# Optimization experiments

Measured on AMD Instinct MI355X. Metric: run time of the kernel, lower is better.

Reference implementation:

```python
import jax, jax.numpy as jnp
import numpy as np

N, E, D, O = 50000, 800000, 128, 128
BN_EPS = 1e-5

def setup_inputs() -> dict:
    key = jax.random.key(0)
    ks = jax.random.split(key, 12)
    s1 = 1.0 / np.sqrt(D)
    s2 = 1.0 / np.sqrt(O)
    return {
        "x": jax.random.normal(ks[0], (N, D), dtype=jnp.float32),
        "edge_index": jax.random.randint(ks[1], (2, E), 0, N, dtype=jnp.int64),
        "batch": jnp.zeros((N,), dtype=jnp.int64),
        "eps": jnp.float32(0.0),  # GINConv train_eps parameter, init 0
        "W1": jax.random.uniform(ks[2], (O, D), jnp.float32, -s1, s1),
        "b1": jax.random.uniform(ks[3], (O,), jnp.float32, -s1, s1),
        "gamma1": jnp.ones((O,), jnp.float32),
        "beta1": jnp.zeros((O,), jnp.float32),
        "W2": jax.random.uniform(ks[4], (O, O), jnp.float32, -s2, s2),
        "b2": jax.random.uniform(ks[5], (O,), jnp.float32, -s2, s2),
        "gamma2": jnp.ones((O,), jnp.float32),
        "beta2": jnp.zeros((O,), jnp.float32),
    }

def _bn(h, gamma, beta):
    # BatchNorm1d training mode: biased variance over nodes
    m = jnp.mean(h, axis=0)
    v = jnp.var(h, axis=0)
    return (h - m) * jax.lax.rsqrt(v + BN_EPS) * gamma + beta

def reference(x, edge_index, batch, eps, W1, b1, gamma1, beta1, W2, b2, gamma2, beta2):
    src, dst = edge_index[0], edge_index[1]
    # sum_{j in N(i)} x_j  (scatter-add over edges)
    agg = jax.ops.segment_sum(x[src], dst, num_segments=N)
    h = (1.0 + eps) * x + agg
    h = jax.nn.relu(_bn(h @ W1.T + b1, gamma1, beta1))
    h = jax.nn.relu(_bn(h @ W2.T + b2, gamma2, beta2))
    return h
```

## Files before the change

kernel.cpp:

```cpp
#include <hip/hip_runtime.h>
#include <hip/hip_bf16.h>

typedef __hip_bfloat16 bf16;
typedef unsigned short u16;
typedef unsigned int u32;
typedef __attribute__((ext_vector_type(8))) short short8;
typedef __attribute__((ext_vector_type(4))) float floatx4;

#define N_NODES 50000
#define N_EDGES 800000
#define DIM 128
#define NB2 1563
#define NB2A 1792
#define CAP2 768
#define T_EDGES 4096
#define NT1 196
#define XCHUNKS 3125
#define WROW 136
#define WIMG (128 * WROW)

__device__ __forceinline__ u16 f2bfbits(float f) {
    bf16 h = __float2bfloat16(f);
    return *(u16*)&h;
}
__device__ __forceinline__ unsigned pack2(float a, float b) {
    return (unsigned)f2bfbits(a) | ((unsigned)f2bfbits(b) << 16);
}
__device__ __forceinline__ float lo2f(u32 u) { u32 v = u << 16; return __builtin_bit_cast(float, v); }
__device__ __forceinline__ float hi2f(u32 u) { u32 v = u & 0xFFFF0000u; return __builtin_bit_cast(float, v); }
__device__ __forceinline__ float b162f(u16 u) { u32 v = (u32)u << 16; return __builtin_bit_cast(float, v); }

__launch_bounds__(256)
__global__ void k1_kernel(const float* __restrict__ x, const int* __restrict__ ei,
                          u32* __restrict__ xb,
                          const float* __restrict__ W1, const float* __restrict__ W2,
                          u16* __restrict__ w1i, u16* __restrict__ w2i,
                          u32* __restrict__ gbuck, int* __restrict__ gcur) {
    __shared__ int hist[NB2A];
    __shared__ int cur[NB2A];
    __shared__ int gbase[NB2A];
    __shared__ int sdet;
    int t = threadIdx.x, bid = blockIdx.x;

    if (bid < NT1) {
        if (t == 0) sdet = 0;
        for (int i = t; i < NB2A; i += 256) { hist[i] = 0; cur[i] = 0; }
        __syncthreads();
        if (t < 64) { if (ei[2 * t + 1] != 0) atomicOr(&sdet, 1); }
        __syncthreads();
        int is64 = (sdet == 0);
        int e0 = bid * T_EDGES;
        int n = N_EDGES - e0; if (n > T_EDGES) n = T_EDGES;
        u32 ed[T_EDGES / 256];
        #pragma unroll
        for (int j = 0; j < T_EDGES / 256; j++) {
            int idx = j * 256 + t;
            if (idx < n) {
                int e = e0 + idx;
                int js = e, jd = N_EDGES + e;
                if (is64) { js = 2 * e; jd = 2 * (N_EDGES + e); }
                u32 p = (u32)ei[js] | ((u32)ei[jd] << 16);
                ed[j] = p;
                atomicAdd(&hist[p >> 21], 1);
            }
        }
        __syncthreads();
        for (int i = t; i < NB2; i += 256) {
            int c = hist[i];
            gbase[i] = c ? atomicAdd(&gcur[i * 16], c) : 0;
        }
        __syncthreads();
        #pragma unroll
        for (int j = 0; j < T_EDGES / 256; j++) {
            int idx = j * 256 + t;
            if (idx < n) {
                u32 p = ed[j];
                int b = p >> 21;
                int pos = gbase[b] + atomicAdd(&cur[b], 1);
                gbuck[(long)b * CAP2 + pos] = p;
            }
        }
    } else if (bid < NT1 + XCHUNKS) {
        int uu = bid - NT1;
        int i = (uu * 256 + t) * 8;
        floatx4 v0 = *(const floatx4*)&x[i];
        floatx4 v1 = *(const floatx4*)&x[i + 4];
        uint4 r;
        r.x = pack2(v0[0], v0[1]); r.y = pack2(v0[2], v0[3]);
        r.z = pack2(v1[0], v1[1]); r.w = pack2(v1[2], v1[3]);
        *(uint4*)&xb[i / 2] = r;
    } else {
        int which = bid - NT1 - XCHUNKS;
        const float* W = which ? W2 : W1;
        u16* wi = which ? w2i : w1i;
        #pragma unroll 4
        for (int j = 0; j < 68; j++) {
            int q = j * 256 + t;
            int r = q / WROW, c = q - r * WROW;
            wi[q] = (c < 128) ? f2bfbits(W[r * 128 + c]) : (u16)0;
        }
    }
}

__launch_bounds__(256)
__global__ void sortagg_kernel(const u32* __restrict__ xb, const u32* __restrict__ gbuck,
                               const int* __restrict__ gcur, const float* __restrict__ epsp,
                               u32* __restrict__ hw) {
    __shared__ u32 sbuf[CAP2];
    __shared__ u16 slist[CAP2];
    __shared__ int cnt[32], offs[32], cur[32];
    int t = threadIdx.x, lane = t & 63, wv = t >> 6;
    int h = lane >> 5, q = lane & 31;
    int b = blockIdx.x;
    int n = gcur[b * 16]; if (n > CAP2) n = CAP2;
    long base = (long)b * CAP2;
    const uint2* xb2 = (const uint2*)xb;

    if (t < 32) { cnt[t] = 0; cur[t] = 0; }
    __syncthreads();
    for (int i = t; i < n; i += 256) {
        u32 p = gbuck[base + i];
        sbuf[i] = p;
        atomicAdd(&cnt[(p >> 16) & 31], 1);
    }
    __syncthreads();
    if (t < 32) {
        int v = cnt[t], pv = v;
        #pragma unroll
        for (int d = 1; d < 32; d <<= 1) { int up = __shfl_up(pv, d); if (t >= d) pv += up; }
        offs[t] = pv - v;
    }
    __syncthreads();
    for (int i = t; i < n; i += 256) {
        u32 p = sbuf[i];
        int d = (p >> 16) & 31;
        int pos = offs[d] + atomicAdd(&cur[d], 1);
        slist[pos] = (u16)(p & 0xFFFF);
    }
    __syncthreads();

    float ep1 = 1.0f + epsp[0];
    for (int p = wv; p < 16; p += 4) {
        int nA = 2 * p, nB = 2 * p + 1;
        int nodeS = b * 32 + 2 * p + h;
        int sOK = nodeS < N_NODES;
        uint2 sS = xb2[(size_t)(sOK ? nodeS : 0) * 32 + q];
        int iA = offs[nA], eA = iA + cnt[nA];
        int iB = offs[nB], eB = iB + cnt[nB];
        float a0 = 0.f, a1 = 0.f, a2 = 0.f, a3 = 0.f;
        float c0 = 0.f, c1 = 0.f, c2 = 0.f, c3 = 0.f;

        while (iA + 8 <= eA && iB + 8 <= eB) {
            int mA[4], mB[4]; uint2 uA[4], uB[4];
            #pragma unroll
            for (int j = 0; j < 4; j++) { mA[j] = slist[iA + 2 * j + h]; mB[j] = slist[iB + 2 * j + h]; }
            #pragma unroll
            for (int j = 0; j < 4; j++) { uA[j] = xb2[(size_t)mA[j] * 32 + q]; uB[j] = xb2[(size_t)mB[j] * 32 + q]; }
            #pragma unroll
            for (int j = 0; j < 4; j++) {
                a0 += lo2f(uA[j].x); a1 += hi2f(uA[j].x); a2 += lo2f(uA[j].y); a3 += hi2f(uA[j].y);
                c0 += lo2f(uB[j].x); c1 += hi2f(uB[j].x); c2 += lo2f(uB[j].y); c3 += hi2f(uB[j].y);
            }
            iA += 8; iB += 8;
        }
        while (iA + 8 <= eA) {
            int mA[4]; uint2 uA[4];
            #pragma unroll
            for (int j = 0; j < 4; j++) mA[j] = slist[iA + 2 * j + h];
            #pragma unroll
            for (int j = 0; j < 4; j++) uA[j] = xb2[(size_t)mA[j] * 32 + q];
            #pragma unroll
            for (int j = 0; j < 4; j++) {
                a0 += lo2f(uA[j].x); a1 += hi2f(uA[j].x); a2 += lo2f(uA[j].y); a3 += hi2f(uA[j].y);
            }
            iA += 8;
        }
        while (iB + 8 <= eB) {
            int mB[4]; uint2 uB[4];
            #pragma unroll
            for (int j = 0; j < 4; j++) mB[j] = slist[iB + 2 * j + h];
            #pragma unroll
            for (int j = 0; j < 4; j++) uB[j] = xb2[(size_t)mB[j] * 32 + q];
            #pragma unroll
            for (int j = 0; j < 4; j++) {
                c0 += lo2f(uB[j].x); c1 += hi2f(uB[j].x); c2 += lo2f(uB[j].y); c3 += hi2f(uB[j].y);
            }
            iB += 8;
        }
        while (iA < eA || iB < eB) {
            int ia0 = iA + h, ia1 = iA + 2 + h, ib0 = iB + h, ib1 = iB + 2 + h;
            int va0 = ia0 < eA, va1 = ia1 < eA, vb0 = ib0 < eB, vb1 = ib1 < eB;
            int mA0 = slist[va0 ? ia0 : 0], mA1 = slist[va1 ? ia1 : 0];
            int mB0 = slist[vb0 ? ib0 : 0], mB1 = slist[vb1 ? ib1 : 0];
            uint2 uA0 = xb2[(size_t)mA0 * 32 + q], uA1 = xb2[(size_t)mA1 * 32 + q];
            uint2 uB0 = xb2[(size_t)mB0 * 32 + q], uB1 = xb2[(size_t)mB1 * 32 + q];
            if (va0) { a0 += lo2f(uA0.x); a1 += hi2f(uA0.x); a2 += lo2f(uA0.y); a3 += hi2f(uA0.y); }
            if (va1) { a0 += lo2f(uA1.x); a1 += hi2f(uA1.x); a2 += lo2f(uA1.y); a3 += hi2f(uA1.y); }
            if (vb0) { c0 += lo2f(uB0.x); c1 += hi2f(uB0.x); c2 += lo2f(uB0.y); c3 += hi2f(uB0.y); }
            if (vb1) { c0 += lo2f(uB1.x); c1 += hi2f(uB1.x); c2 += lo2f(uB1.y); c3 += hi2f(uB1.y); }
            iA += 4; iB += 4;
        }
        if (sOK) {
            if (h == 0) {
                a0 += ep1 * lo2f(sS.x); a1 += ep1 * hi2f(sS.x);
                a2 += ep1 * lo2f(sS.y); a3 += ep1 * hi2f(sS.y);
            } else {
                c0 += ep1 * lo2f(sS.x); c1 += ep1 * hi2f(sS.x);
                c2 += ep1 * lo2f(sS.y); c3 += ep1 * hi2f(sS.y);
            }
        }
        a0 += __shfl_xor(a0, 32); a1 += __shfl_xor(a1, 32);
        a2 += __shfl_xor(a2, 32); a3 += __shfl_xor(a3, 32);
        c0 += __shfl_xor(c0, 32); c1 += __shfl_xor(c1, 32);
        c2 += __shfl_xor(c2, 32); c3 += __shfl_xor(c3, 32);
        float r0 = h ? c0 : a0, r1 = h ? c1 : a1, r2 = h ? c2 : a2, r3 = h ? c3 : a3;
        if (sOK) {
            uint2 w; w.x = pack2(r0, r1); w.y = pack2(r2, r3);
            *(uint2*)&hw[(size_t)nodeS * 64 + 2 * q] = w;
        }
    }
}

template<int TRANSFORM>
__launch_bounds__(256)
__global__ void gemm_mfma(const u16* __restrict__ Ap, const u16* __restrict__ wimg,
                          const float* __restrict__ bias,
                          const float* __restrict__ gamma, const float* __restrict__ beta,
                          const float* __restrict__ gstat,
                          u16* __restrict__ Yp, float* __restrict__ ostat) {
    __shared__ u16 sW[WIMG];
    __shared__ float sScale[128], sShift[128], sBias[128], sSum[128], sSq[128];
    int t = threadIdx.x, lane = t & 63, wv = t >> 6;

    #pragma unroll
    for (int it = 0; it < 9; it++) {
        int q = it * 256 + t;
        if (q < WIMG / 8) *(uint4*)&sW[q * 8] = ((const uint4*)wimg)[q];
    }
    if (t < 128) {
        sSum[t] = 0.f; sSq[t] = 0.f; sBias[t] = bias[t];
        if (TRANSFORM) {
            float m = gstat[t * 16] * (1.0f / N_NODES);
            float v = fmaxf(gstat[t * 16 + 8] * (1.0f / N_NODES) - m * m, 0.0f);
            float rs = rsqrtf(v + 1e-5f);
            float sc = gamma[t] * rs;
            sScale[t] = sc;
            sShift[t] = beta[t] - m * sc;
        }
    }
    __syncthreads();

    int col0 = lane & 15, quad = lane >> 4;
    int row0 = blockIdx.x * 128 + wv * 32;

    short8 afr[2][4];
    #pragma unroll
    for (int tt = 0; tt < 2; tt++) {
        int mrow = row0 + tt * 16 + col0;
        if (mrow > N_NODES - 1) mrow = N_NODES - 1;
        #pragma unroll
        for (int ks = 0; ks < 4; ks++)
            afr[tt][ks] = *(const short8*)&Ap[mrow * DIM + ks * 32 + quad * 8];
    }
    if (TRANSFORM) {
        #pragma unroll
        for (int tt = 0; tt < 2; tt++)
            #pragma unroll
            for (int ks = 0; ks < 4; ks++) {
                int kb = ks * 32 + quad * 8;
                short8 a = afr[tt][ks], r;
                #pragma unroll
                for (int j = 0; j < 8; j++) {
                    float f = b162f((u16)a[j]);
                    r[j] = (short)f2bfbits(fmaxf(fmaf(f, sScale[kb + j], sShift[kb + j]), 0.f));
                }
                afr[tt][ks] = r;
            }
    }

    floatx4 acc[2][8];
    #pragma unroll
    for (int tt = 0; tt < 2; tt++)
        #pragma unroll
        for (int nt = 0; nt < 8; nt++) acc[tt][nt] = (floatx4){0.f, 0.f, 0.f, 0.f};
    #pragma unroll
    for (int ks = 0; ks < 4; ks++)
        #pragma unroll
        for (int nt = 0; nt < 8; nt++) {
            short8 bfr = *(const short8*)&sW[(nt * 16 + col0) * WROW + ks * 32 + quad * 8];
            acc[0][nt] = __builtin_amdgcn_mfma_f32_16x16x32_bf16(afr[0][ks], bfr, acc[0][nt], 0, 0, 0);
            acc[1][nt] = __builtin_amdgcn_mfma_f32_16x16x32_bf16(afr[1][ks], bfr, acc[1][nt], 0, 0, 0);
        }

    #pragma unroll
    for (int tt = 0; tt < 2; tt++) {
        int rtile = row0 + tt * 16;
        if (rtile >= N_NODES) break;
        #pragma unroll
        for (int nt = 0; nt < 8; nt++) {
            int col = nt * 16 + col0;
            float bb = sBias[col];
            float o0 = acc[tt][nt][0] + bb, o1 = acc[tt][nt][1] + bb;
            float o2 = acc[tt][nt][2] + bb, o3 = acc[tt][nt][3] + bb;
            int rbase = rtile + quad * 4;
            Yp[(rbase + 0) * DIM + col] = f2bfbits(o0);
            Yp[(rbase + 1) * DIM + col] = f2bfbits(o1);
            Yp[(rbase + 2) * DIM + col] = f2bfbits(o2);
            Yp[(rbase + 3) * DIM + col] = f2bfbits(o3);
            float s = o0 + o1 + o2 + o3;
            float q = o0 * o0 + o1 * o1 + o2 * o2 + o3 * o3;
            s += __shfl_xor(s, 16); s += __shfl_xor(s, 32);
            q += __shfl_xor(q, 16); q += __shfl_xor(q, 32);
            if (quad == 0) { atomicAdd(&sSum[col], s); atomicAdd(&sSq[col], q); }
        }
    }
    __syncthreads();
    if (t < 128) {
        atomicAdd(&ostat[t * 16], sSum[t]);
        atomicAdd(&ostat[t * 16 + 8], sSq[t]);
    }
}

__global__ void output_kernel(const u32* __restrict__ Y,
                              const float* __restrict__ gstat,
                              const float* __restrict__ gamma, const float* __restrict__ beta,
                              float* __restrict__ out) {
    __shared__ float sScale[128], sShift[128];
    int t = threadIdx.x;
    if (t < 128) {
        float m = gstat[t * 16] * (1.0f / N_NODES);
        float v = fmaxf(gstat[t * 16 + 8] * (1.0f / N_NODES) - m * m, 0.0f);
        float rs = rsqrtf(v + 1e-5f);
        float sc = gamma[t] * rs;
        sScale[t] = sc;
        sShift[t] = beta[t] - m * sc;
    }
    __syncthreads();
    int i = (blockIdx.x * 256 + t) * 8;
    int c = i & 127;
    uint4 v = *(const uint4*)&Y[i / 2];
    u32 w[4] = {v.x, v.y, v.z, v.w};
    floatx4 o0, o1;
    #pragma unroll
    for (int j = 0; j < 4; j++) {
        float lo = lo2f(w[j]), hi = hi2f(w[j]);
        float r0 = fmaxf(fmaf(lo, sScale[c + 2 * j],     sShift[c + 2 * j]),     0.f);
        float r1 = fmaxf(fmaf(hi, sScale[c + 2 * j + 1], sShift[c + 2 * j + 1]), 0.f);
        if (j < 2) { o0[2 * j] = r0; o0[2 * j + 1] = r1; }
        else       { o1[2 * (j - 2)] = r0; o1[2 * (j - 2) + 1] = r1; }
    }
    *(floatx4*)&out[i] = o0;
    *(floatx4*)&out[i + 4] = o1;
}

extern "C" void kernel_launch(void* const* d_in, const int* in_sizes, int n_in,
                              void* d_out, int out_size, void* d_ws, size_t ws_size,
                              hipStream_t stream) {
    const float* x   = (const float*)d_in[0];
    const int* eraw  = (const int*)d_in[1];
    const float* eps = (const float*)d_in[3];
    const float* W1  = (const float*)d_in[4];
    const float* b1  = (const float*)d_in[5];
    const float* g1  = (const float*)d_in[6];
    const float* be1 = (const float*)d_in[7];
    const float* W2  = (const float*)d_in[8];
    const float* b2  = (const float*)d_in[9];
    const float* g2  = (const float*)d_in[10];
    const float* be2 = (const float*)d_in[11];

    char* ws = (char*)d_ws;
    size_t off = 0;
    u32* xb = (u32*)(ws + off);          off += (size_t)N_NODES * DIM * 2;
    u32* h1 = (u32*)(ws + off);          off += (size_t)N_NODES * DIM * 2;
    u16* y1 = (u16*)(ws + off);          off += (size_t)N_NODES * DIM * 2;
    u16* y2 = (u16*)(ws + off);          off += (size_t)N_NODES * DIM * 2;
    float* stats = (float*)(ws + off);   off += 4096 * 4;
    float* st1 = stats;
    float* st2 = stats + 2048;
    u16* w1i = (u16*)(ws + off);         off += (size_t)WIMG * 2;
    u16* w2i = (u16*)(ws + off);         off += (size_t)WIMG * 2;
    u32* gbuck = (u32*)(ws + off);       off += (size_t)NB2 * CAP2 * 4;
    int* gcur = (int*)(ws + off);        off += (size_t)((NB2 * 16 + 255) & ~255) * 4;

    hipMemsetAsync(gcur, 0, (size_t)NB2 * 16 * 4, stream);
    hipMemsetAsync(stats, 0, 4096 * 4, stream);

    k1_kernel<<<NT1 + XCHUNKS + 2, 256, 0, stream>>>(x, eraw, xb, W1, W2, w1i, w2i, gbuck, gcur);
    sortagg_kernel<<<NB2, 256, 0, stream>>>(xb, gbuck, gcur, eps, h1);

    const int gemmGrid = (N_NODES + 127) / 128;
    gemm_mfma<0><<<gemmGrid, 256, 0, stream>>>((const u16*)h1, w1i, b1,
                                               nullptr, nullptr, nullptr, y1, st1);
    gemm_mfma<1><<<gemmGrid, 256, 0, stream>>>(y1, w2i, b2,
                                               g1, be1, st1, y2, st2);
    output_kernel<<<N_NODES * DIM / (8 * 256), 256, 0, stream>>>((const u32*)y2, st2,
                                                                 g2, be2, (float*)d_out);
}
```

Measured before the change: 231.0 us.

## Replace atomic fixed-capacity bucketing with deterministic histogram-scan-scatter counting sort

Measured after the change: 243.0 us. +5.2%, slower.

```diff
diff --git a/kernel.cpp b/kernel.cpp
--- a/kernel.cpp
+++ b/kernel.cpp
@@ -11,13 +11,13 @@
 #define N_EDGES 800000
 #define DIM 128
 #define NB2 1563
-#define NB2A 1792
-#define CAP2 768
+#define HP 2048
 #define T_EDGES 4096
 #define NT1 196
 #define XCHUNKS 3125
 #define WROW 136
 #define WIMG (128 * WROW)
+#define SCAP 768
 
 __device__ __forceinline__ u16 f2bfbits(float f) {
     bf16 h = __float2bfloat16(f);
@@ -35,50 +35,46 @@
                           u32* __restrict__ xb,
                           const float* __restrict__ W1, const float* __restrict__ W2,
                           u16* __restrict__ w1i, u16* __restrict__ w2i,
-                          u32* __restrict__ gbuck, int* __restrict__ gcur) {
-    __shared__ int hist[NB2A];
-    __shared__ int cur[NB2A];
-    __shared__ int gbase[NB2A];
-    __shared__ int sdet;
+                          u32* __restrict__ H) {
     int t = threadIdx.x, bid = blockIdx.x;
 
     if (bid < NT1) {
+        __shared__ int hist[HP];
+        __shared__ int sdet;
         if (t == 0) sdet = 0;
-        for (int i = t; i < NB2A; i += 256) { hist[i] = 0; cur[i] = 0; }
+        #pragma unroll
+        for (int j = 0; j < HP / 256; j++) hist[j * 256 + t] = 0;
         __syncthreads();
         if (t < 64) { if (ei[2 * t + 1] != 0) atomicOr(&sdet, 1); }
         __syncthreads();
         int is64 = (sdet == 0);
         int e0 = bid * T_EDGES;
         int n = N_EDGES - e0; if (n > T_EDGES) n = T_EDGES;
-        u32 ed[T_EDGES / 256];
-        #pragma unroll
-        for (int j = 0; j < T_EDGES / 256; j++) {
-            int idx = j * 256 + t;
-            if (idx < n) {
-                int e = e0 + idx;
-                int js = e, jd = N_EDGES + e;
-                if (is64) { js = 2 * e; jd = 2 * (N_EDGES + e); }
-                u32 p = (u32)ei[js] | ((u32)ei[jd] << 16);
-                ed[j] = p;
-                atomicAdd(&hist[p >> 21], 1);
+        if (n == T_EDGES) {
+            #pragma unroll
+            for (int j = 0; j < T_EDGES / 256; j++) {
+                int e = e0 + j * 256 + t;
+                int jd = is64 ? 2 * (N_EDGES + e) : (N_EDGES + e);
+                u32 d = (u32)ei[jd];
+                atomicAdd(&hist[d >> 5], 1);
+            }
+        } else {
+            #pragma unroll
+            for (int j = 0; j < T_EDGES / 256; j++) {
+                int idx = j * 256 + t;
+                if (idx < n) {
+                    int e = e0 + idx;
+                    int jd = is64 ? 2 * (N_EDGES + e) : (N_EDGES + e);
+                    u32 d = (u32)ei[jd];
+                    atomicAdd(&hist[d >> 5], 1);
+                }
             }
         }
         __syncthreads();
-        for (int i = t; i < NB2; i += 256) {
-            int c = hist[i];
-            gbase[i] = c ? atomicAdd(&gcur[i * 16], c) : 0;
-        }
-        __syncthreads();
-        #pragma unroll
-        for (int j = 0; j < T_EDGES / 256; j++) {
-            int idx = j * 256 + t;
-            if (idx < n) {
-                u32 p = ed[j];
-                int b = p >> 21;
-                int pos = gbase[b] + atomicAdd(&cur[b], 1);
-                gbuck[(long)b * CAP2 + pos] = p;
-            }
+        #pragma unroll
+        for (int j = 0; j < 4; j++) {
+            int i = j * 256 + t;
+            H[bid * (HP / 2) + i] = (u32)hist[2 * i] | ((u32)hist[2 * i + 1] << 16);
         }
     } else if (bid < NT1 + XCHUNKS) {
         int uu = bid - NT1;
@@ -103,17 +99,86 @@
 }
 
 __launch_bounds__(256)
+__global__ void scatter_kernel(const int* __restrict__ ei, const u32* __restrict__ H,
+                               u32* __restrict__ gbuck, u32* __restrict__ bsG) {
+    __shared__ u32 bsL[HP];
+    __shared__ int curL[HP];
+    __shared__ int waveTot[4];
+    __shared__ int sdet;
+    int t = threadIdx.x, lane = t & 63, wv = t >> 6;
+    int tile = blockIdx.x;
+
+    u32 acc4[4] = {0, 0, 0, 0}, cp4[4] = {0, 0, 0, 0};
+    const uint4* Hr = (const uint4*)H;
+    for (int r = 0; r < NT1; r++) {
+        if (r == tile) { cp4[0] = acc4[0]; cp4[1] = acc4[1]; cp4[2] = acc4[2]; cp4[3] = acc4[3]; }
+        uint4 h = Hr[r * 256 + t];
+        acc4[0] += h.x; acc4[1] += h.y; acc4[2] += h.z; acc4[3] += h.w;
+    }
+    u32 a[8], c8[8];
+    #pragma unroll
+    for (int k = 0; k < 4; k++) {
+        a[2 * k] = acc4[k] & 0xFFFF; a[2 * k + 1] = acc4[k] >> 16;
+        c8[2 * k] = cp4[k] & 0xFFFF; c8[2 * k + 1] = cp4[k] >> 16;
+    }
+    u32 run = 0, excl[8];
+    #pragma unroll
+    for (int k = 0; k < 8; k++) { excl[k] = run; run += a[k]; }
+    int v = (int)run;
+    int vi = v;
+    #pragma unroll
+    for (int d = 1; d < 64; d <<= 1) { int up = __shfl_up(vi, d); if (lane >= d) vi += up; }
+    if (lane == 63) waveTot[wv] = vi;
+    if (t == 0) sdet = 0;
+    __syncthreads();
+    int woff = 0;
+    #pragma unroll
+    for (int w = 0; w < 3; w++) if (w < wv) woff += waveTot[w];
+    int tb = woff + vi - v;
+    #pragma unroll
+    for (int k = 0; k < 8; k++) {
+        int b = t * 8 + k;
+        bsL[b] = (u32)tb + excl[k] + c8[k];
+        curL[b] = 0;
+    }
+    if (t < 64) { if (ei[2 * t + 1] != 0) atomicOr(&sdet, 1); }
+    __syncthreads();
+
+    if (tile == 0) {
+        for (int i = t; i < NB2; i += 256) bsG[i] = bsL[i];
+        if (t == 0) bsG[NB2] = N_EDGES;
+    }
+
+    int is64 = (sdet == 0);
+    int e0 = tile * T_EDGES;
+    int n = N_EDGES - e0; if (n > T_EDGES) n = T_EDGES;
+    #pragma unroll
+    for (int j = 0; j < T_EDGES / 256; j++) {
+        int idx = j * 256 + t;
+        if (idx < n) {
+            int e = e0 + idx;
+            int js = e, jd = N_EDGES + e;
+            if (is64) { js = 2 * e; jd = 2 * (N_EDGES + e); }
+            u32 p = (u32)ei[js] | ((u32)ei[jd] << 16);
+            int b = p >> 21;
+            int pos = atomicAdd(&curL[b], 1);
+            gbuck[bsL[b] + pos] = p;
+        }
+    }
+}
+
+__launch_bounds__(256)
 __global__ void sortagg_kernel(const u32* __restrict__ xb, const u32* __restrict__ gbuck,
-                               const int* __restrict__ gcur, const float* __restrict__ epsp,
+                               const u32* __restrict__ bsG, const float* __restrict__ epsp,
                                u32* __restrict__ hw) {
-    __shared__ u32 sbuf[CAP2];
-    __shared__ u16 slist[CAP2];
+    __shared__ u32 sbuf[SCAP];
+    __shared__ u16 slist[SCAP];
     __shared__ int cnt[32], offs[32], cur[32];
     int t = threadIdx.x, lane = t & 63, wv = t >> 6;
     int h = lane >> 5, q = lane & 31;
     int b = blockIdx.x;
-    int n = gcur[b * 16]; if (n > CAP2) n = CAP2;
-    long base = (long)b * CAP2;
+    u32 base = bsG[b];
+    int n = (int)(bsG[b + 1] - base); if (n > SCAP) n = SCAP;
     const uint2* xb2 = (const uint2*)xb;
 
     if (t < 32) { cnt[t] = 0; cur[t] = 0; }
@@ -379,14 +444,15 @@
     float* st2 = stats + 2048;
     u16* w1i = (u16*)(ws + off);         off += (size_t)WIMG * 2;
     u16* w2i = (u16*)(ws + off);         off += (size_t)WIMG * 2;
-    u32* gbuck = (u32*)(ws + off);       off += (size_t)NB2 * CAP2 * 4;
-    int* gcur = (int*)(ws + off);        off += (size_t)((NB2 * 16 + 255) & ~255) * 4;
-
-    hipMemsetAsync(gcur, 0, (size_t)NB2 * 16 * 4, stream);
+    u32* H = (u32*)(ws + off);           off += (size_t)NT1 * (HP / 2) * 4;
+    u32* gbuck = (u32*)(ws + off);       off += (size_t)N_EDGES * 4;
+    u32* bsG = (u32*)(ws + off);         off += 2048 * 4;
+
     hipMemsetAsync(stats, 0, 4096 * 4, stream);
 
-    k1_kernel<<<NT1 + XCHUNKS + 2, 256, 0, stream>>>(x, eraw, xb, W1, W2, w1i, w2i, gbuck, gcur);
-    sortagg_kernel<<<NB2, 256, 0, stream>>>(xb, gbuck, gcur, eps, h1);
+    k1_kernel<<<NT1 + XCHUNKS + 2, 256, 0, stream>>>(x, eraw, xb, W1, W2, w1i, w2i, H);
+    scatter_kernel<<<NT1, 256, 0, stream>>>(eraw, H, gbuck, bsG);
+    sortagg_kernel<<<NB2, 256, 0, stream>>>(xb, gbuck, bsG, eps, h1);
 
     const int gemmGrid = (N_NODES + 127) / 128;
     gemm_mfma<0><<<gemmGrid, 256, 0, stream>>>((const u16*)h1, w1i, b1,
```
